# Performance work log

Measured on AMD Instinct MI355X. Metric: run time of the kernel, lower is better.

## Reference

```python
import jax, jax.numpy as jnp
import numpy as np

TAU = 0.5  # matches init_kwargs tau
EPS = 1e-8  # torch CosineSimilarity eps


def setup_inputs() -> dict:
    key = jax.random.key(0)
    k1, k2 = jax.random.split(key)
    B, D = 4096, 256
    return {
        "z_orig": jax.random.normal(k1, (B, D), dtype=jnp.float32),
        "z_augment": jax.random.normal(k2, (B, D), dtype=jnp.float32),
    }


def reference(z_orig, z_augment):
    B = z_orig.shape[0]
    N = 2 * B
    # collect_z = cat([z_augment, z_orig])  -> [2B, D]
    z = jnp.concatenate([z_augment, z_orig], axis=0)
    # cosine similarity matrix via L2 normalize + matmul
    zn = z / jnp.maximum(jnp.linalg.norm(z, axis=-1, keepdims=True), EPS)
    S = zn @ zn.T  # [2B, 2B]
    # positives: diag offsets +B and -B
    pos = jnp.concatenate([jnp.diagonal(S, B), jnp.diagonal(S, -B)])[:, None]  # [2B, 1]
    # negatives: everything except main diag and the +/-B diagonals.
    # Static indices (shape-dependent only), computed in numpy at trace time.
    mask = ~((np.eye(N, k=B) + np.eye(N, k=-B) + np.eye(N)).astype(bool))
    flat_idx = jnp.asarray(np.nonzero(mask.reshape(-1))[0])  # [2B*(2B-2)]
    neg = S.reshape(-1)[flat_idx].reshape(N, N - 2)  # row-major order matches torch boolean mask
    logits = jnp.concatenate([pos, neg], axis=1) / TAU  # [2B, 2B-1]
    # CrossEntropy with label 0 for every row, reduction='sum', then / 2B
    loss = -jax.nn.log_softmax(logits, axis=-1)[:, 0]
    return jnp.sum(loss) / N
```

## Files before the change

kernel.cpp:

```cpp
#include <hip/hip_runtime.h>
#include <hip/hip_bf16.h>

typedef __attribute__((ext_vector_type(4))) float f32x4;
typedef __attribute__((ext_vector_type(4))) int   i32x4;
typedef __attribute__((ext_vector_type(8))) int   i32x8;

#define N_ROWS 8192
#define B_HALF 4096
#define NUT   2080
#define EXP2C4 0.01127105500694503f
#define SCL1   0x7F7F7F7Fu

#define WS_ZN       0
#define WS_ROWACC   2097152
#define WS_POS      2129920
#define WS_DIAG     2162688
#define WS_ACC      2195456
#define WS_CNT      2195460

__device__ __forceinline__ float fexp2(float x) {
#if __has_builtin(__builtin_amdgcn_exp2f)
    return __builtin_amdgcn_exp2f(x);
#else
    return exp2f(x);
#endif
}

__device__ __forceinline__ unsigned int q4(float x) {
    float a = fabsf(x);
    unsigned int s = (__float_as_uint(x) >> 31) << 3;
    unsigned int c = a < 0.25f ? 0u : a < 0.75f ? 1u : a < 1.25f ? 2u
                   : a < 1.75f ? 3u : a < 2.5f  ? 4u : a < 3.5f  ? 5u
                   : a < 5.0f  ? 6u : 7u;
    return c | s;
}

__device__ __forceinline__ i32x8 widen(i32x4 v) {
    return (i32x8){v.x, v.y, v.z, v.w, 0, 0, 0, 0};
}

__device__ __forceinline__ float dpp_rowsum16(float x) {
    x += __int_as_float(__builtin_amdgcn_update_dpp(
             0, __float_as_int(x), 0x111, 0xF, 0xF, true));
    x += __int_as_float(__builtin_amdgcn_update_dpp(
             0, __float_as_int(x), 0x112, 0xF, 0xF, true));
    x += __int_as_float(__builtin_amdgcn_update_dpp(
             0, __float_as_int(x), 0x114, 0xF, 0xF, true));
    x += __int_as_float(__builtin_amdgcn_update_dpp(
             0, __float_as_int(x), 0x118, 0xF, 0xF, true));
    return x;
}

__device__ __forceinline__ void async_copy16(const void* g, void* l) {
    __builtin_amdgcn_global_load_lds(
        (const __attribute__((address_space(1))) unsigned int*)g,
        (__attribute__((address_space(3))) unsigned int*)l,
        16, 0, 0);
}

__global__ __launch_bounds__(256) void normalize_k(
    const float* __restrict__ z_orig, const float* __restrict__ z_aug,
    unsigned char* __restrict__ zn, float* __restrict__ rowAcc,
    float* __restrict__ accum, unsigned int* __restrict__ cnt)
{
    if (blockIdx.x == 0 && threadIdx.x == 0) { *accum = 0.0f; *cnt = 0u; }
    const int row  = blockIdx.x * 4 + (threadIdx.x >> 6);
    const int lane = threadIdx.x & 63;
    if (lane == 0) rowAcc[row] = 0.0f;
    const float* src = (row < B_HALF) ? (z_aug  + (size_t)row * 256)
                                      : (z_orig + (size_t)(row - B_HALF) * 256);
    float4 v = ((const float4*)src)[lane];
    float ss = v.x*v.x + v.y*v.y + v.z*v.z + v.w*v.w;
    #pragma unroll
    for (int m = 1; m < 64; m <<= 1) ss += __shfl_xor(ss, m);
    float inv = 16.0f / fmaxf(sqrtf(ss), 1e-8f);
    unsigned int pk = q4(v.x * inv) | (q4(v.y * inv) << 4)
                    | (q4(v.z * inv) << 8) | (q4(v.w * inv) << 12);
    const int addr = ((row >> 4) << 11) | ((lane >> 5) << 10) | ((row & 15) << 6)
                   | (((lane >> 3) & 3) << 4) | ((lane & 7) << 1);
    *(unsigned short*)(zn + addr) = (unsigned short)pk;
}

__global__ __launch_bounds__(256, 4) void tile_k(
    const unsigned char* __restrict__ zn,
    float* __restrict__ rowAcc,
    float* __restrict__ posv,
    float* __restrict__ diagE)
{
    __shared__ unsigned char As[16384];
    __shared__ unsigned char Bs[16384];

    const int bid = blockIdx.x;
    int rb = (int)((129.0f - sqrtf(16641.0f - 8.0f * (float)bid)) * 0.5f);
    rb = rb < 0 ? 0 : (rb > 63 ? 63 : rb);
    while ((rb + 1) * (129 - (rb + 1)) / 2 <= bid) ++rb;
    while (rb * (129 - rb) / 2 > bid) --rb;
    const int cb = rb + (bid - rb * (129 - rb) / 2);

    const int t      = threadIdx.x;
    const int lane   = t & 63;
    const int w      = t >> 6;
    const int wy     = w >> 1;
    const int wx     = w & 1;
    const int lane15 = lane & 15;
    const int quad   = lane >> 4;
    const int rowBase = rb * 128;
    const int colBase = cb * 128;

    {
        const int off = t * 16;
        const unsigned char* gA = zn + (size_t)rb * 16384;
        #pragma unroll
        for (int s = 0; s < 4; ++s)
            async_copy16(gA + s * 4096 + off, As + s * 4096 + off);
        if (cb != rb) {
            const unsigned char* gB = zn + (size_t)cb * 16384;
            #pragma unroll
            for (int s = 0; s < 4; ++s)
                async_copy16(gB + s * 4096 + off, Bs + s * 4096 + off);
        }
    }
    __syncthreads();
    const unsigned char* Bb = (cb == rb) ? As : Bs;

    const int laneOff = lane15 * 64 + quad * 16;
    f32x4 acc[4][4];
    #pragma unroll
    for (int i = 0; i < 4; ++i)
        #pragma unroll
        for (int j = 0; j < 4; ++j)
            acc[i][j] = (f32x4){0.f, 0.f, 0.f, 0.f};

    #pragma unroll
    for (int ks = 0; ks < 2; ++ks) {
        i32x4 a[4], b[4];
        #pragma unroll
        for (int mi = 0; mi < 4; ++mi)
            a[mi] = *(const i32x4*)(As + (wy * 4 + mi) * 2048 + ks * 1024 + laneOff);
        #pragma unroll
        for (int ni = 0; ni < 4; ++ni)
            b[ni] = *(const i32x4*)(Bb + (wx * 4 + ni) * 2048 + ks * 1024 + laneOff);
        #pragma unroll
        for (int mi = 0; mi < 4; ++mi)
            #pragma unroll
            for (int ni = 0; ni < 4; ++ni)
                acc[mi][ni] = __builtin_amdgcn_mfma_scale_f32_16x16x128_f8f6f4(
                    widen(a[mi]), widen(b[ni]), acc[mi][ni],
                    4, 4, 0, SCL1, 0, SCL1);
    }

    const bool diagLane = (wy == wx) && ((lane15 >> 2) == quad);
    const int  rsel = lane15 & 3;
    if (cb == rb && diagLane) {
        #pragma unroll
        for (int mi = 0; mi < 4; ++mi) {
            int grow = rowBase + wy * 64 + mi * 16 + lane15;
            diagE[grow] = fexp2(acc[mi][mi][rsel] * EXP2C4);
        }
    }
    if (cb == rb + 32 && diagLane) {
        #pragma unroll
        for (int mi = 0; mi < 4; ++mi) {
            int grow = rowBase + wy * 64 + mi * 16 + lane15;
            float v = acc[mi][mi][rsel];
            posv[grow] = v;
            posv[grow + B_HALF] = v;
        }
    }

    #pragma unroll
    for (int mi = 0; mi < 4; ++mi)
        #pragma unroll
        for (int ni = 0; ni < 4; ++ni)
            #pragma unroll
            for (int r = 0; r < 4; ++r)
                acc[mi][ni][r] = fexp2(acc[mi][ni][r] * EXP2C4);

    #pragma unroll
    for (int mi = 0; mi < 4; ++mi)
        #pragma unroll
        for (int r = 0; r < 4; ++r) {
            float s = acc[mi][0][r] + acc[mi][1][r] + acc[mi][2][r] + acc[mi][3][r];
            s = dpp_rowsum16(s);
            if (lane15 == 15)
                atomicAdd(&rowAcc[rowBase + wy * 64 + mi * 16 + quad * 4 + r], s);
        }

    if (cb != rb) {
        #pragma unroll
        for (int ni = 0; ni < 4; ++ni) {
            float s = 0.0f;
            #pragma unroll
            for (int mi = 0; mi < 4; ++mi)
                s += acc[mi][ni][0] + acc[mi][ni][1] + acc[mi][ni][2] + acc[mi][ni][3];
            s += __shfl_xor(s, 16);
            s += __shfl_xor(s, 32);
            if (quad == 0)
                atomicAdd(&rowAcc[colBase + wx * 64 + ni * 16 + lane15], s);
        }
    }
}

__global__ __launch_bounds__(256) void loss_k(
    const float* __restrict__ rowAcc, const float* __restrict__ posv,
    const float* __restrict__ diagE, float* __restrict__ accum,
    unsigned int* __restrict__ cnt, float* __restrict__ out)
{
    const int i = blockIdx.x * 256 + threadIdx.x;
    float s = rowAcc[i] - diagE[i];
    float loss = __logf(s) - posv[i] * 0.0078125f;

    #pragma unroll
    for (int m = 1; m < 64; m <<= 1) loss += __shfl_xor(loss, m);
    __shared__ float red[4];
    if ((threadIdx.x & 63) == 0) red[threadIdx.x >> 6] = loss;
    __syncthreads();
    if (threadIdx.x == 0) {
        float bs = red[0] + red[1] + red[2] + red[3];
        atomicAdd(accum, bs);
        __threadfence();
        unsigned int old = atomicAdd(cnt, 1u);
        if (old == 31u) {
            __threadfence();
            float total = atomicAdd(accum, 0.0f);
            out[0] = total * (1.0f / (float)N_ROWS);
        }
    }
}

extern "C" void kernel_launch(void* const* d_in, const int* in_sizes, int n_in,
                              void* d_out, int out_size, void* d_ws, size_t ws_size,
                              hipStream_t stream) {
    const float* z_orig = (const float*)d_in[0];
    const float* z_aug  = (const float*)d_in[1];
    char* ws = (char*)d_ws;
    unsigned char* zn   = (unsigned char*)(ws + WS_ZN);
    float* rowAcc       = (float*)(ws + WS_ROWACC);
    float* posv         = (float*)(ws + WS_POS);
    float* diagE        = (float*)(ws + WS_DIAG);
    float* accum        = (float*)(ws + WS_ACC);
    unsigned int* cnt   = (unsigned int*)(ws + WS_CNT);

    normalize_k<<<N_ROWS / 4, 256, 0, stream>>>(z_orig, z_aug, zn, rowAcc, accum, cnt);
    tile_k<<<NUT, 256, 0, stream>>>(zn, rowAcc, posv, diagE);
    loss_k<<<N_ROWS / 256, 256, 0, stream>>>(rowAcc, posv, diagE, accum, cnt,
                                             (float*)d_out);
}
```

Before: 89.11 us.

## Process two column tiles per block sharing one A row tile in LDS

Each 512-thread block now handles one row block and two adjacent upper-triangle column blocks, so the A tile is loaded once and reused for both. The triangular block-index decode with sqrt is replaced by a 2D grid (32x64), with blocks past the triangle exiting early. This is meant to cut redundant global/LDS loads of A and the index math. In exchange, about half the grid does no work, LDS per block grows, and occupancy changes.

```diff
diff --git a/kernel.cpp b/kernel.cpp
--- a/kernel.cpp
+++ b/kernel.cpp
@@ -7,7 +7,6 @@
 
 #define N_ROWS 8192
 #define B_HALF 4096
-#define NUT   2080
 #define EXP2C4 0.01127105500694503f
 #define SCL1   0x7F7F7F7Fu
 
@@ -81,49 +80,57 @@
     *(unsigned short*)(zn + addr) = (unsigned short)pk;
 }
 
-__global__ __launch_bounds__(256, 4) void tile_k(
+__global__ __launch_bounds__(512, 2) void tile_k(
     const unsigned char* __restrict__ zn,
     float* __restrict__ rowAcc,
     float* __restrict__ posv,
     float* __restrict__ diagE)
 {
     __shared__ unsigned char As[16384];
-    __shared__ unsigned char Bs[16384];
-
-    const int bid = blockIdx.x;
-    int rb = (int)((129.0f - sqrtf(16641.0f - 8.0f * (float)bid)) * 0.5f);
-    rb = rb < 0 ? 0 : (rb > 63 ? 63 : rb);
-    while ((rb + 1) * (129 - (rb + 1)) / 2 <= bid) ++rb;
-    while (rb * (129 - rb) / 2 > bid) --rb;
-    const int cb = rb + (bid - rb * (129 - rb) / 2);
+    __shared__ unsigned char Bs[32768];
+
+    const int rb  = blockIdx.y;
+    const int cb0 = rb + 2 * (int)blockIdx.x;
+    if (cb0 > 63) return;
+    const bool have1 = (cb0 + 1 <= 63);
 
     const int t      = threadIdx.x;
     const int lane   = t & 63;
     const int w      = t >> 6;
-    const int wy     = w >> 1;
-    const int wx     = w & 1;
+    const int wy     = w >> 2;
+    const int wxg    = w & 3;
+    const int cb     = cb0 + (wxg >> 1);
+    const int wx     = wxg & 1;
     const int lane15 = lane & 15;
     const int quad   = lane >> 4;
     const int rowBase = rb * 128;
-    const int colBase = cb * 128;
+    const bool diagLane = (wy == wx) && ((lane15 >> 2) == quad);
+    const int  rsel = lane15 & 3;
 
     {
         const int off = t * 16;
         const unsigned char* gA = zn + (size_t)rb * 16384;
         #pragma unroll
-        for (int s = 0; s < 4; ++s)
-            async_copy16(gA + s * 4096 + off, As + s * 4096 + off);
-        if (cb != rb) {
-            const unsigned char* gB = zn + (size_t)cb * 16384;
-            #pragma unroll
-            for (int s = 0; s < 4; ++s)
-                async_copy16(gB + s * 4096 + off, Bs + s * 4096 + off);
+        for (int s = 0; s < 2; ++s)
+            async_copy16(gA + s * 8192 + off, As + s * 8192 + off);
+        const unsigned char* gB = zn + (size_t)cb0 * 16384;
+        #pragma unroll
+        for (int s = 0; s < 2; ++s)
+            async_copy16(gB + s * 8192 + off, Bs + s * 8192 + off);
+        if (have1) {
+            #pragma unroll
+            for (int s = 0; s < 2; ++s)
+                async_copy16(gB + 16384 + s * 8192 + off,
+                             Bs + 16384 + s * 8192 + off);
         }
     }
     __syncthreads();
-    const unsigned char* Bb = (cb == rb) ? As : Bs;
+
+    if (cb > 63) return;
 
     const int laneOff = lane15 * 64 + quad * 16;
+    const unsigned char* Bw = Bs + wxg * 8192;
+
     f32x4 acc[4][4];
     #pragma unroll
     for (int i = 0; i < 4; ++i)
@@ -139,7 +146,7 @@
             a[mi] = *(const i32x4*)(As + (wy * 4 + mi) * 2048 + ks * 1024 + laneOff);
         #pragma unroll
         for (int ni = 0; ni < 4; ++ni)
-            b[ni] = *(const i32x4*)(Bb + (wx * 4 + ni) * 2048 + ks * 1024 + laneOff);
+            b[ni] = *(const i32x4*)(Bw + ni * 2048 + ks * 1024 + laneOff);
         #pragma unroll
         for (int mi = 0; mi < 4; ++mi)
             #pragma unroll
@@ -149,8 +156,7 @@
                     4, 4, 0, SCL1, 0, SCL1);
     }
 
-    const bool diagLane = (wy == wx) && ((lane15 >> 2) == quad);
-    const int  rsel = lane15 & 3;
+    const int colBase = cb * 128;
     if (cb == rb && diagLane) {
         #pragma unroll
         for (int mi = 0; mi < 4; ++mi) {
@@ -242,7 +248,7 @@
     unsigned int* cnt   = (unsigned int*)(ws + WS_CNT);
 
     normalize_k<<<N_ROWS / 4, 256, 0, stream>>>(z_orig, z_aug, zn, rowAcc, accum, cnt);
-    tile_k<<<NUT, 256, 0, stream>>>(zn, rowAcc, posv, diagE);
+    tile_k<<<dim3(32, 64), 512, 0, stream>>>(zn, rowAcc, posv, diagE);
     loss_k<<<N_ROWS / 256, 256, 0, stream>>>(rowAcc, posv, diagE, accum, cnt,
                                              (float*)d_out);
 }
```

Result: slower. 100.2 us (+12.4%).
